# Performance work log

Hardware: AMD Instinct MI355X
Metric: run time of the kernel (lower is better)

Reference implementation:

```python
import jax, jax.numpy as jnp
import numpy as np

S, B, C, H, E = 4096, 2, 256, 8, 131072
CC = C // H


def setup_inputs() -> dict:
    key = jax.random.key(0)
    ks = jax.random.split(key, 12)
    sc = 0.02
    inp = {
        "x": jax.random.normal(ks[0], (S, B, C), jnp.float32),
        "q_id": jax.random.randint(ks[1], (E,), 0, S, jnp.int32),
        "k_id": jax.random.randint(ks[2], (E,), 0, S, jnp.int32),
        "Wq": jax.random.normal(ks[3], (C, C), jnp.float32) * sc,
        "bq": jnp.zeros((C,), jnp.float32),
        "Wk": jax.random.normal(ks[4], (C, C), jnp.float32) * sc,
        "bk": jnp.zeros((C,), jnp.float32),
        "Wv": jax.random.normal(ks[5], (C, C), jnp.float32) * sc,
        "bv": jnp.zeros((C,), jnp.float32),
        "Wx": jax.random.normal(ks[6], (C, C), jnp.float32) * sc,
        "bx": jnp.zeros((C,), jnp.float32),
    }
    return inp


def reference(x, q_id, k_id, Wq, bq, Wk, bk, Wv, bv, Wx, bx):
    s, b, c = x.shape
    cc = c // H
    # qkv projections (torch Linear: x @ W.T + b)
    q = (x @ Wq.T + bq).reshape(s, b, H, cc)
    k = (x @ Wk.T + bk).reshape(s, b, H, cc)
    v = (x @ Wv.T + bv).reshape(s, b, H, cc)
    # per-edge scores: gather along sequence axis by edge ids
    qk = jnp.einsum('ebhc,ebhc->ebh', q[q_id], k[k_id])[..., None]  # [E,b,h,1]
    qk = qk / jnp.sqrt(jnp.asarray(cc, x.dtype))
    eqk = jnp.exp(qk - jnp.max(qk))  # global max, as in original
    # scatter-add softmax normalizer and weighted sum over edges
    d = jnp.zeros((s, b, H, 1), x.dtype).at[q_id].add(eqk)
    out = jnp.zeros((s, b, H, cc), x.dtype).at[q_id].add(eqk * v[k_id])
    out = (out / d).reshape(s, b, c)
    return out @ Wx.T + bx
```

## Files before the change

kernel.cpp:

```cpp
#include <hip/hip_runtime.h>

constexpr int S_  = 4096;
constexpr int B_  = 2;
constexpr int C_  = 256;
constexpr int H_  = 8;
constexpr int E_  = 131072;
constexpr int CC_ = 32;
constexpr int MR  = S_ * B_;

typedef __attribute__((ext_vector_type(8))) short bf16x8_t;
typedef __attribute__((ext_vector_type(4))) float f32x4_t;

__device__ __forceinline__ unsigned short f2bf(float f) {
    unsigned int u = __float_as_uint(f);
    u += 0x7fffu + ((u >> 16) & 1u);
    return (unsigned short)(u >> 16);
}
__device__ __forceinline__ float bflo(unsigned int u) { return __uint_as_float(u << 16); }
__device__ __forceinline__ float bfhi(unsigned int u) { return __uint_as_float(u & 0xffff0000u); }

__device__ __forceinline__ void cast8(const float* __restrict__ src, unsigned short* __restrict__ dst, int i) {
    const float4* s = (const float4*)src + (size_t)i * 2;
    float4 a = s[0], b = s[1];
    uint4 o;
    o.x = (unsigned)f2bf(a.x) | ((unsigned)f2bf(a.y) << 16);
    o.y = (unsigned)f2bf(a.z) | ((unsigned)f2bf(a.w) << 16);
    o.z = (unsigned)f2bf(b.x) | ((unsigned)f2bf(b.y) << 16);
    o.w = (unsigned)f2bf(b.z) | ((unsigned)f2bf(b.w) << 16);
    *((uint4*)dst + i) = o;
}


__global__ __launch_bounds__(256) void prep_kernel(
        const int* __restrict__ q_id, int* __restrict__ count,
        const float* __restrict__ x, unsigned short* __restrict__ xb,
        const float* __restrict__ Wq, const float* __restrict__ Wk,
        const float* __restrict__ Wv, const float* __restrict__ Wx,
        unsigned short* __restrict__ Wb) {
    const int bid = blockIdx.x, tid = threadIdx.x;
    if (bid < 512) {
        atomicAdd(&count[q_id[bid * 256 + tid]], 1);
    } else if (bid < 1536) {
        cast8(x, xb, (bid - 512) * 256 + tid);
    } else {
        int idx = bid - 1536;
        int z = idx >> 5;
        const float* src = (z == 0) ? Wq : (z == 1) ? Wk : (z == 2) ? Wv : Wx;
        cast8(src, Wb + (size_t)z * (C_ * C_), (idx & 31) * 256 + tid);
    }
}


__global__ __launch_bounds__(1024) void scan_kernel(const int* __restrict__ count,
                                                    int* __restrict__ base,
                                                    int* __restrict__ cursor) {
    __shared__ int wsums[16];
    const int t = threadIdx.x, lane = t & 63, w = t >> 6;
    int c0 = count[4 * t + 0], c1 = count[4 * t + 1];
    int c2 = count[4 * t + 2], c3 = count[4 * t + 3];
    int tsum = c0 + c1 + c2 + c3;
    int x = tsum;
#pragma unroll
    for (int off = 1; off < 64; off <<= 1) {
        int y = __shfl_up(x, off);
        if (lane >= off) x += y;
    }
    if (lane == 63) wsums[w] = x;
    __syncthreads();
    if (t == 0) {
        int run = 0;
#pragma unroll
        for (int i = 0; i < 16; ++i) { int v = wsums[i]; wsums[i] = run; run += v; }
        base[S_] = run;
    }
    __syncthreads();
    int excl = x - tsum + wsums[w];
    int b0 = excl, b1 = b0 + c0, b2 = b1 + c1, b3 = b2 + c2;
    base[4 * t + 0] = b0; base[4 * t + 1] = b1;
    base[4 * t + 2] = b2; base[4 * t + 3] = b3;
    cursor[4 * t + 0] = b0; cursor[4 * t + 1] = b1;
    cursor[4 * t + 2] = b2; cursor[4 * t + 3] = b3;
}


__global__ __launch_bounds__(256) void scatter_qkv_kernel(
        const int* __restrict__ q_id, const int* __restrict__ k_id,
        int* __restrict__ cursor, int* __restrict__ koff_sorted,
        const unsigned short* __restrict__ xb, const unsigned short* __restrict__ Wb,
        const float* __restrict__ bq, const float* __restrict__ bk, const float* __restrict__ bv,
        unsigned short* __restrict__ qb, unsigned short* __restrict__ kvb) {
    __shared__ __align__(16) unsigned short As[64][264];
    const int bid = blockIdx.x, tid = threadIdx.x;
    if (bid < 512) {
        int e = bid * 256 + tid;
        int pos = atomicAdd(&cursor[q_id[e]], 1);
        koff_sorted[pos] = k_id[e] << 10;
        return;
    }
    const int u = bid - 512;
    const int nb = u % 12, mg = u / 12;
    const int lane = tid & 63, wave = tid >> 6;
    const int l16 = lane & 15, quad = lane >> 4;
    const int z = nb >> 2;
    const int colz = ((nb & 3) << 6) + (wave << 4);

    const unsigned short* Wrow = Wb + (size_t)z * (C_ * C_) + (size_t)(colz + l16) * C_;
    bf16x8_t breg[8];
#pragma unroll
    for (int ks = 0; ks < 8; ++ks)
        breg[ks] = *(const bf16x8_t*)(Wrow + ks * 32 + quad * 8);

    const float* bias = (z == 0) ? bq : (z == 1) ? bk : bv;
    const float bcol = bias[colz + l16];
    unsigned short* ob = (z == 0) ? qb : kvb;
    const int ostr = (z == 0) ? 256 : 512;
    const int ocol = ((z == 2) ? 256 : 0) + colz + l16;

    const int c0 = (mg * 128) / 43, c1 = ((mg + 1) * 128) / 43;
    for (int c = c0; c < c1; ++c) {
        const int mbase = c * 64;
        __syncthreads();
#pragma unroll
        for (int it = 0; it < 8; ++it) {
            int l = it * 256 + tid;
            int r = l >> 5, cc = (l & 31) << 3;
            *(uint4*)&As[r][cc] = *(const uint4*)&xb[(size_t)(mbase + r) * C_ + cc];
        }
        __syncthreads();
#pragma unroll
        for (int mt = 0; mt < 4; ++mt) {
            f32x4_t acc = {0.f, 0.f, 0.f, 0.f};
#pragma unroll
            for (int ks = 0; ks < 8; ++ks) {
                bf16x8_t a = *(const bf16x8_t*)&As[mt * 16 + l16][ks * 32 + quad * 8];
                acc = __builtin_amdgcn_mfma_f32_16x16x32_bf16(a, breg[ks], acc, 0, 0, 0);
            }
            const int row0 = mbase + mt * 16 + quad * 4;
#pragma unroll
            for (int r = 0; r < 4; ++r)
                ob[(size_t)(row0 + r) * ostr + ocol] = f2bf(acc[r] + bcol);
        }
    }
}


__global__ __launch_bounds__(256) void attn_edge(
        const unsigned short* __restrict__ qb, const unsigned short* __restrict__ kvb,
        const int* __restrict__ base, const int* __restrict__ koff,
        unsigned short* __restrict__ attnb) {
    __shared__ float red[2][64][9];
    const int lane = threadIdx.x & 63;
    const int wave = threadIdx.x >> 6;
    const int rw = wave >> 1, part = wave & 1;
    const int s = blockIdx.x * 2 + rw;
    const int half = lane >> 5, hl = lane & 31;
    const int e0 = __builtin_amdgcn_readfirstlane(base[s]);
    const int e1 = __builtin_amdgcn_readfirstlane(base[s + 1]);

    const uint4 qq = *((const uint4*)(qb + (size_t)(s * 2 + half) * C_) + hl);
    const float q0 = bflo(qq.x), q1 = bfhi(qq.x), q2 = bflo(qq.y), q3 = bfhi(qq.y);
    const float q4 = bflo(qq.z), q5 = bfhi(qq.z), q6 = bflo(qq.w), q7 = bfhi(qq.w);

    float a0 = 0.f, a1 = 0.f, a2 = 0.f, a3 = 0.f, a4 = 0.f, a5 = 0.f, a6 = 0.f, a7 = 0.f;
    float wsum = 0.f;
    const float scale = 0.17677669529663687f;

    auto edge = [&](const uint4& kk, const uint4& vv) {
        float p = q0 * bflo(kk.x) + q1 * bfhi(kk.x)
                + q2 * bflo(kk.y) + q3 * bfhi(kk.y)
                + q4 * bflo(kk.z) + q5 * bfhi(kk.z)
                + q6 * bflo(kk.w) + q7 * bfhi(kk.w);
        p += __shfl_xor(p, 1);
        p += __shfl_xor(p, 2);
        const float w = __expf(p * scale);
        a0 = fmaf(w, bflo(vv.x), a0); a1 = fmaf(w, bfhi(vv.x), a1);
        a2 = fmaf(w, bflo(vv.y), a2); a3 = fmaf(w, bfhi(vv.y), a3);
        a4 = fmaf(w, bflo(vv.z), a4); a5 = fmaf(w, bfhi(vv.z), a5);
        a6 = fmaf(w, bflo(vv.w), a6); a7 = fmaf(w, bfhi(vv.w), a7);
        wsum += w;
    };
    auto fetch = [&](int my, int t, uint4& kk, uint4& vv) {
        int o = __builtin_amdgcn_readlane(my, part + 2 * t);
        const uint4* p = (const uint4*)(kvb + o + half * 512);
        kk = p[hl]; vv = p[32 + hl];
    };

    for (int b0 = e0; b0 < e1; b0 += 64) {
        const int m = min(64, e1 - b0);
        const int my = koff[b0 + ((lane < m) ? lane : 0)];
        const int nm = (m > part) ? ((m - part + 1) >> 1) : 0;
        uint4 kka = {}, vva = {}, kkb = {}, vvb = {};
        if (nm > 0) fetch(my, 0, kka, vva);
        if (nm > 1) fetch(my, 1, kkb, vvb);
        int t = 0;
        for (; t + 3 < nm; t += 2) {
            edge(kka, vva);
            fetch(my, t + 2, kka, vva);
            edge(kkb, vvb);
            fetch(my, t + 3, kkb, vvb);
        }
        if (t < nm)     edge(kka, vva);
        if (t + 1 < nm) edge(kkb, vvb);
        if (t + 2 < nm) { fetch(my, t + 2, kka, vva); edge(kka, vva); }
    }

    if (part == 1) {
        float* r = red[rw][lane];
        r[0] = a0; r[1] = a1; r[2] = a2; r[3] = a3;
        r[4] = a4; r[5] = a5; r[6] = a6; r[7] = a7; r[8] = wsum;
    }
    __syncthreads();
    if (part == 0) {
        const float* r = red[rw][lane];
        a0 += r[0]; a1 += r[1]; a2 += r[2]; a3 += r[3];
        a4 += r[4]; a5 += r[5]; a6 += r[6]; a7 += r[7]; wsum += r[8];
        const float inv = 1.0f / wsum;
        uint4 o;
        o.x = (unsigned)f2bf(a0 * inv) | ((unsigned)f2bf(a1 * inv) << 16);
        o.y = (unsigned)f2bf(a2 * inv) | ((unsigned)f2bf(a3 * inv) << 16);
        o.z = (unsigned)f2bf(a4 * inv) | ((unsigned)f2bf(a5 * inv) << 16);
        o.w = (unsigned)f2bf(a6 * inv) | ((unsigned)f2bf(a7 * inv) << 16);
        *((uint4*)(attnb + (size_t)(s * 2 + half) * C_) + hl) = o;
    }
}


__global__ __launch_bounds__(256) void gemm_proj(
        const unsigned short* __restrict__ attnb, const unsigned short* __restrict__ Wxb,
        const float* __restrict__ bx, float* __restrict__ out) {
    __shared__ __align__(16) unsigned short As[64][264];
    const int tid = threadIdx.x;
    const int nb = blockIdx.x & 3, mg = blockIdx.x >> 2;
    const int lane = tid & 63, wave = tid >> 6;
    const int l16 = lane & 15, quad = lane >> 4;
    const int colz = (nb << 6) + (wave << 4);

    const unsigned short* Wrow = Wxb + (size_t)(colz + l16) * C_;
    bf16x8_t breg[8];
#pragma unroll
    for (int ks = 0; ks < 8; ++ks)
        breg[ks] = *(const bf16x8_t*)(Wrow + ks * 32 + quad * 8);
    const float bcol = bx[colz + l16];
    const int ocol = colz + l16;

    const int mbase = mg * 64;
#pragma unroll
    for (int it = 0; it < 8; ++it) {
        int l = it * 256 + tid;
        int r = l >> 5, cc = (l & 31) << 3;
        *(uint4*)&As[r][cc] = *(const uint4*)&attnb[(size_t)(mbase + r) * C_ + cc];
    }
    __syncthreads();
#pragma unroll
    for (int mt = 0; mt < 4; ++mt) {
        f32x4_t acc = {0.f, 0.f, 0.f, 0.f};
#pragma unroll
        for (int ks = 0; ks < 8; ++ks) {
            bf16x8_t a = *(const bf16x8_t*)&As[mt * 16 + l16][ks * 32 + quad * 8];
            acc = __builtin_amdgcn_mfma_f32_16x16x32_bf16(a, breg[ks], acc, 0, 0, 0);
        }
        const int row0 = mbase + mt * 16 + quad * 4;
#pragma unroll
        for (int r = 0; r < 4; ++r)
            out[(size_t)(row0 + r) * C_ + ocol] = acc[r] + bcol;
    }
}


extern "C" void kernel_launch(void* const* d_in, const int* in_sizes, int n_in,
                              void* d_out, int out_size, void* d_ws, size_t ws_size,
                              hipStream_t stream) {
    const float* x  = (const float*)d_in[0];
    const int* q_id = (const int*)d_in[1];
    const int* k_id = (const int*)d_in[2];
    const float* Wq = (const float*)d_in[3];
    const float* bq = (const float*)d_in[4];
    const float* Wk = (const float*)d_in[5];
    const float* bk = (const float*)d_in[6];
    const float* Wv = (const float*)d_in[7];
    const float* bv = (const float*)d_in[8];
    const float* Wx = (const float*)d_in[9];
    const float* bx = (const float*)d_in[10];
    float* out = (float*)d_out;

    char* ws = (char*)d_ws;
    unsigned short* xb    = (unsigned short*)ws;                 ws += (size_t)MR * C_ * 2;
    unsigned short* qb    = (unsigned short*)ws;                 ws += (size_t)MR * C_ * 2;
    unsigned short* kvb   = (unsigned short*)ws;                 ws += (size_t)MR * 512 * 2;
    unsigned short* attnb = (unsigned short*)ws;                 ws += (size_t)MR * C_ * 2;
    unsigned short* Wb    = (unsigned short*)ws;                 ws += (size_t)4 * C_ * C_ * 2;
    int* count       = (int*)ws;                                 ws += S_ * 4;
    int* base        = (int*)ws;                                 ws += (S_ + 1) * 4;
    int* cursor      = (int*)ws;                                 ws += S_ * 4;
    int* koff_sorted = (int*)ws;

    hipMemsetAsync(count, 0, S_ * sizeof(int), stream);
    prep_kernel<<<1664, 256, 0, stream>>>(q_id, count, x, xb, Wq, Wk, Wv, Wx, Wb);
    scan_kernel<<<1, 1024, 0, stream>>>(count, base, cursor);
    scatter_qkv_kernel<<<1028, 256, 0, stream>>>(q_id, k_id, cursor, koff_sorted,
                                                 xb, Wb, bq, bk, bv, qb, kvb);
    attn_edge<<<S_ / 2, 256, 0, stream>>>(qb, kvb, base, koff_sorted, attnb);
    gemm_proj<<<512, 256, 0, stream>>>(attnb, Wb + (size_t)3 * C_ * C_, bx, out);
}
```

Baseline: 147.8 us.

## Fuse Q/K/V projections per tile and deepen edge-gather prefetch to four

The QKV projection blocks now each take one 64-row tile and compute all three projections from a single staged A tile, holding Q, K and V weight fragments in registers. Before, 516 persistent blocks looped over tiles for one projection each. The GEMM blocks now come first in the grid, and the scatter blocks move after them. The attention edge loop now keeps four K/V fetches in flight instead of two, to hide gather latency. This raises register pressure in both kernels, which may lower occupancy.

```diff
diff --git a/kernel.cpp b/kernel.cpp
--- a/kernel.cpp
+++ b/kernel.cpp
@@ -91,54 +91,71 @@
         unsigned short* __restrict__ qb, unsigned short* __restrict__ kvb) {
     __shared__ __align__(16) unsigned short As[64][264];
     const int bid = blockIdx.x, tid = threadIdx.x;
-    if (bid < 512) {
-        int e = bid * 256 + tid;
+    if (bid >= 512) {
+        int e = (bid - 512) * 256 + tid;
         int pos = atomicAdd(&cursor[q_id[e]], 1);
         koff_sorted[pos] = k_id[e] << 10;
         return;
     }
-    const int u = bid - 512;
-    const int nb = u % 12, mg = u / 12;
+    const int nb = bid & 3, mg = bid >> 2;
     const int lane = tid & 63, wave = tid >> 6;
     const int l16 = lane & 15, quad = lane >> 4;
-    const int z = nb >> 2;
-    const int colz = ((nb & 3) << 6) + (wave << 4);
-
-    const unsigned short* Wrow = Wb + (size_t)z * (C_ * C_) + (size_t)(colz + l16) * C_;
-    bf16x8_t breg[8];
-#pragma unroll
-    for (int ks = 0; ks < 8; ++ks)
-        breg[ks] = *(const bf16x8_t*)(Wrow + ks * 32 + quad * 8);
-
-    const float* bias = (z == 0) ? bq : (z == 1) ? bk : bv;
-    const float bcol = bias[colz + l16];
-    unsigned short* ob = (z == 0) ? qb : kvb;
-    const int ostr = (z == 0) ? 256 : 512;
-    const int ocol = ((z == 2) ? 256 : 0) + colz + l16;
-
-    const int c0 = (mg * 128) / 43, c1 = ((mg + 1) * 128) / 43;
-    for (int c = c0; c < c1; ++c) {
-        const int mbase = c * 64;
-        __syncthreads();
-#pragma unroll
-        for (int it = 0; it < 8; ++it) {
-            int l = it * 256 + tid;
-            int r = l >> 5, cc = (l & 31) << 3;
-            *(uint4*)&As[r][cc] = *(const uint4*)&xb[(size_t)(mbase + r) * C_ + cc];
-        }
-        __syncthreads();
-#pragma unroll
-        for (int mt = 0; mt < 4; ++mt) {
+    const int colz = (nb << 6) + (wave << 4);
+
+    bf16x8_t breg[3][8];
+#pragma unroll
+    for (int z = 0; z < 3; ++z) {
+        const unsigned short* Wrow = Wb + (size_t)z * (C_ * C_) + (size_t)(colz + l16) * C_;
+#pragma unroll
+        for (int ks = 0; ks < 8; ++ks)
+            breg[z][ks] = *(const bf16x8_t*)(Wrow + ks * 32 + quad * 8);
+    }
+    const float bc0 = bq[colz + l16];
+    const float bc1 = bk[colz + l16];
+    const float bc2 = bv[colz + l16];
+
+    const int mbase = mg * 64;
+#pragma unroll
+    for (int it = 0; it < 8; ++it) {
+        int l = it * 256 + tid;
+        int r = l >> 5, cc = (l & 31) << 3;
+        *(uint4*)&As[r][cc] = *(const uint4*)&xb[(size_t)(mbase + r) * C_ + cc];
+    }
+    __syncthreads();
+
+#pragma unroll
+    for (int mt = 0; mt < 4; ++mt) {
+        bf16x8_t a[8];
+#pragma unroll
+        for (int ks = 0; ks < 8; ++ks)
+            a[ks] = *(const bf16x8_t*)&As[mt * 16 + l16][ks * 32 + quad * 8];
+        const int row0 = mbase + mt * 16 + quad * 4;
+        {
             f32x4_t acc = {0.f, 0.f, 0.f, 0.f};
 #pragma unroll
-            for (int ks = 0; ks < 8; ++ks) {
-                bf16x8_t a = *(const bf16x8_t*)&As[mt * 16 + l16][ks * 32 + quad * 8];
-                acc = __builtin_amdgcn_mfma_f32_16x16x32_bf16(a, breg[ks], acc, 0, 0, 0);
-            }
-            const int row0 = mbase + mt * 16 + quad * 4;
+            for (int ks = 0; ks < 8; ++ks)
+                acc = __builtin_amdgcn_mfma_f32_16x16x32_bf16(a[ks], breg[0][ks], acc, 0, 0, 0);
 #pragma unroll
             for (int r = 0; r < 4; ++r)
-                ob[(size_t)(row0 + r) * ostr + ocol] = f2bf(acc[r] + bcol);
+                qb[(size_t)(row0 + r) * 256 + colz + l16] = f2bf(acc[r] + bc0);
+        }
+        {
+            f32x4_t acc = {0.f, 0.f, 0.f, 0.f};
+#pragma unroll
+            for (int ks = 0; ks < 8; ++ks)
+                acc = __builtin_amdgcn_mfma_f32_16x16x32_bf16(a[ks], breg[1][ks], acc, 0, 0, 0);
+#pragma unroll
+            for (int r = 0; r < 4; ++r)
+                kvb[(size_t)(row0 + r) * 512 + colz + l16] = f2bf(acc[r] + bc1);
+        }
+        {
+            f32x4_t acc = {0.f, 0.f, 0.f, 0.f};
+#pragma unroll
+            for (int ks = 0; ks < 8; ++ks)
+                acc = __builtin_amdgcn_mfma_f32_16x16x32_bf16(a[ks], breg[2][ks], acc, 0, 0, 0);
+#pragma unroll
+            for (int r = 0; r < 4; ++r)
+                kvb[(size_t)(row0 + r) * 512 + 256 + colz + l16] = f2bf(acc[r] + bc2);
         }
     }
 }
@@ -189,19 +206,27 @@
         const int m = min(64, e1 - b0);
         const int my = koff[b0 + ((lane < m) ? lane : 0)];
         const int nm = (m > part) ? ((m - part + 1) >> 1) : 0;
-        uint4 kka = {}, vva = {}, kkb = {}, vvb = {};
-        if (nm > 0) fetch(my, 0, kka, vva);
-        if (nm > 1) fetch(my, 1, kkb, vvb);
+        uint4 k0 = {}, v0 = {}, k1 = {}, v1 = {};
+        uint4 k2 = {}, v2 = {}, k3 = {}, v3 = {};
+        if (nm > 0) fetch(my, 0, k0, v0);
+        if (nm > 1) fetch(my, 1, k1, v1);
+        if (nm > 2) fetch(my, 2, k2, v2);
+        if (nm > 3) fetch(my, 3, k3, v3);
         int t = 0;
-        for (; t + 3 < nm; t += 2) {
-            edge(kka, vva);
-            fetch(my, t + 2, kka, vva);
-            edge(kkb, vvb);
-            fetch(my, t + 3, kkb, vvb);
-        }
-        if (t < nm)     edge(kka, vva);
-        if (t + 1 < nm) edge(kkb, vvb);
-        if (t + 2 < nm) { fetch(my, t + 2, kka, vva); edge(kka, vva); }
+        for (; t + 7 < nm; t += 4) {
+            edge(k0, v0); fetch(my, t + 4, k0, v0);
+            edge(k1, v1); fetch(my, t + 5, k1, v1);
+            edge(k2, v2); fetch(my, t + 6, k2, v2);
+            edge(k3, v3); fetch(my, t + 7, k3, v3);
+        }
+        const int rem = nm - t;
+        if (rem > 0) { edge(k0, v0); if (rem > 4) fetch(my, t + 4, k0, v0); }
+        if (rem > 1) { edge(k1, v1); if (rem > 5) fetch(my, t + 5, k1, v1); }
+        if (rem > 2) { edge(k2, v2); if (rem > 6) fetch(my, t + 6, k2, v2); }
+        if (rem > 3) edge(k3, v3);
+        if (rem > 4) edge(k0, v0);
+        if (rem > 5) edge(k1, v1);
+        if (rem > 6) edge(k2, v2);
     }
 
     if (part == 1) {
@@ -297,7 +322,7 @@
     hipMemsetAsync(count, 0, S_ * sizeof(int), stream);
     prep_kernel<<<1664, 256, 0, stream>>>(q_id, count, x, xb, Wq, Wk, Wv, Wx, Wb);
     scan_kernel<<<1, 1024, 0, stream>>>(count, base, cursor);
-    scatter_qkv_kernel<<<1028, 256, 0, stream>>>(q_id, k_id, cursor, koff_sorted,
+    scatter_qkv_kernel<<<1024, 256, 0, stream>>>(q_id, k_id, cursor, koff_sorted,
                                                  xb, Wb, bq, bk, bv, qb, kvb);
     attn_edge<<<S_ / 2, 256, 0, stream>>>(qb, kvb, base, koff_sorted, attnb);
     gemm_proj<<<512, 256, 0, stream>>>(attnb, Wb + (size_t)3 * C_ * C_, bx, out);
```

New measurement: 145.0 us. No clear change (-1.9%).
